# Optimization experiments

Hardware: AMD Instinct MI355X
Metric: run time of the kernel (lower is better)

## Reference

```python
import jax, jax.numpy as jnp
import numpy as np

K_DEPTH = 3
JAC_A = 1.0  # alpha (Jacobi a)
JAC_B = 1.0  # beta  (Jacobi b)


def jacobi_filter(sig, gammas):
    """Polynomial graph filter g(sigma) = sum_k gamma_k * P_k^{(a,b)}(sigma),
    Jacobi recurrence applied elementwise (Sigma is diagonal spectrum), domain [-1,1],
    fixed inner scalings (fixI=True => alphas=1)."""
    a, b = JAC_A, JAC_B
    xs = [jnp.ones_like(sig)]
    # L = 1
    coef1 = (a - b) / 2.0
    coef2 = (a + b + 2.0) / 2.0
    xs.append(coef1 * xs[0] + coef2 * sig * xs[0])
    for L in range(2, K_DEPTH + 1):
        cl = 2.0 * L * (L + a + b) * (2 * L - 2 + a + b)
        c1 = (2 * L + a + b - 1) * (2 * L + a + b) * (2 * L + a + b - 2)
        c2 = (2 * L + a + b - 1) * (a * a - b * b)
        c3 = 2.0 * (L - 1 + a) * (L - 1 + b) * (2 * L + a + b)
        xs.append((c1 / cl) * sig * xs[-1] - (c2 / cl) * xs[-1] - (c3 / cl) * xs[-2])
    basis = jnp.stack(xs, axis=0)  # [K+1, B, H, L, d]
    return jnp.einsum('k,kbhld->bhld', gammas, basis)


def setup_inputs() -> dict:
    key = jax.random.key(0)
    ks = jax.random.split(key, 7)
    B, L, Ha, Hs, d = 4, 2048, 4, 4, 64
    mk = lambda k, H: jax.random.normal(k, (B, L, H, d), dtype=jnp.float32)
    return {
        'U': mk(ks[0], Ha),
        'Sigma': mk(ks[1], Ha),
        'V': mk(ks[2], Ha),
        'values': mk(ks[3], Ha),
        'queries_softmax': mk(ks[4], Hs),
        'keys_softmax': mk(ks[5], Hs),
        'values_softmax': mk(ks[6], Hs),
        'gammas': jnp.ones((K_DEPTH + 1,), dtype=jnp.float32),
    }


def reference(U, Sigma, V, values, queries_softmax, keys_softmax, values_softmax, gammas):
    d_k = U.shape[-1]
    # ---- AGF (SVD) heads ----
    Uh = jax.nn.softmax(jnp.transpose(U, (0, 2, 1, 3)), axis=-1)        # [B,H,L,d]
    Vt = jax.nn.softmax(jnp.transpose(V, (0, 2, 3, 1)), axis=-1)        # [B,H,d,L]
    vals = jnp.transpose(values, (0, 2, 1, 3))                           # [B,H,L,d]
    sig = jax.nn.sigmoid(jnp.transpose(Sigma, (0, 2, 1, 3)))             # [B,H,L,d]
    gf = jacobi_filter(sig, gammas)                                       # [B,H,L,d]
    kv = jnp.einsum('bhdl,bhle->bhde', Vt, vals)                          # [B,H,d,d]
    out_agf = jnp.einsum('bhld,bhde->bhle', Uh * gf, kv)                  # [B,H,L,d]
    out_agf = jnp.transpose(out_agf, (0, 2, 1, 3))                        # [B,L,H,d]
    # ---- orthogonality loss ----
    eye = jnp.eye(d_k, dtype=Uh.dtype)
    sym_u = jnp.einsum('bhld,bhle->bhde', Uh, Uh) - eye
    sym_v = jnp.einsum('bhdl,bhel->bhde', Vt, Vt) - eye
    ortho_loss = jnp.mean(jnp.abs(sym_u), axis=(1, 2, 3)) + jnp.mean(jnp.abs(sym_v), axis=(1, 2, 3))
    # ---- softmax (flash) heads ----
    q = jnp.transpose(queries_softmax, (0, 2, 1, 3))
    k = jnp.transpose(keys_softmax, (0, 2, 1, 3))
    v = jnp.transpose(values_softmax, (0, 2, 1, 3))
    scores = jnp.einsum('bhld,bhsd->bhls', q, k) / jnp.sqrt(jnp.asarray(d_k, q.dtype))
    attn = jax.nn.softmax(scores, axis=-1)
    out_sm = jnp.einsum('bhls,bhsd->bhld', attn, v)
    out_sm = jnp.transpose(out_sm, (0, 2, 1, 3))                          # [B,L,H,d]
    out = jnp.concatenate([out_agf, out_sm], axis=2)                      # [B,L,2H,d]
    return out, ortho_loss
```

## Files before the change

kernel.cpp:

```cpp
#include <hip/hip_runtime.h>
#include <hip/hip_bf16.h>

#define BB 4
#define SEQ 2048
#define NH 4
#define D 64
#define NPAIR 16
#define HOUT 8
#define LOSS_BASE ((size_t)BB * SEQ * HOUT * D)

#define N_PART   (4 * 16 * 3 * 4096)
#define OFF_SPART N_PART
#define N_SPART  (16 * 32 * 64)
#define OFF_LPART (OFF_SPART + N_SPART)
#define N_LPART  (4 * 16 * 2048)
#define OFF_F32_END (OFF_LPART + N_LPART)
#define USZ ((size_t)16 * 2048 * 64)

typedef __attribute__((ext_vector_type(8))) short bf16x8;
typedef __attribute__((ext_vector_type(4))) float f32x4;
typedef __attribute__((ext_vector_type(8))) unsigned short us8;
typedef __attribute__((ext_vector_type(4))) unsigned short us4;

__device__ __forceinline__ unsigned short f2bf(float x) {
    union { float f; unsigned u; } v; v.f = x;
    unsigned r = v.u + 0x7fffu + ((v.u >> 16) & 1u);
    return (unsigned short)(r >> 16);
}
__device__ __forceinline__ float bf2f(unsigned short u) {
    union { unsigned u; float f; } v; v.u = ((unsigned)u) << 16; return v.f;
}
__device__ __forceinline__ unsigned cvt_pk_bf16(float lo, float hi) {
    unsigned r;
    asm("v_cvt_pk_bf16_f32 %0, %1, %2" : "=v"(r) : "v"(lo), "v"(hi));
    return r;
}
__device__ __forceinline__ void load16(const float* p, float* v) {
    const float4* q = (const float4*)p;
    float4 a = q[0], b = q[1], c = q[2], d = q[3];
    v[0]=a.x; v[1]=a.y; v[2]=a.z; v[3]=a.w;
    v[4]=b.x; v[5]=b.y; v[6]=b.z; v[7]=b.w;
    v[8]=c.x; v[9]=c.y; v[10]=c.z; v[11]=c.w;
    v[12]=d.x; v[13]=d.y; v[14]=d.z; v[15]=d.w;
}
__device__ __forceinline__ void wr_bf16x16(unsigned short* dst, const float* v) {
    unsigned w[8];
#pragma unroll
    for (int i = 0; i < 8; i++) w[i] = cvt_pk_bf16(v[2 * i], v[2 * i + 1]);
    *(uint4*)dst = make_uint4(w[0], w[1], w[2], w[3]);
    *(uint4*)(dst + 8) = make_uint4(w[4], w[5], w[6], w[7]);
}

__global__ __launch_bounds__(256) void prep(const float* __restrict__ U, const float* __restrict__ Sg,
                                            const float* __restrict__ Vagf, const float* __restrict__ vals,
                                            const float* __restrict__ Ksm, const float* __restrict__ Vsm,
                                            const float* __restrict__ gam,
                                            float* __restrict__ ws, unsigned short* __restrict__ usb,
                                            float* __restrict__ out) {
    int lt = blockIdx.x, p = blockIdx.y, stage = blockIdx.z;
    int b = p >> 2, h = p & 3;
    int tid = threadIdx.x;
    int r = tid >> 2;
    int c0 = (tid & 3) * 16;
    __shared__ float T[64][68];
    unsigned short* Khi   = usb;
    unsigned short* VbfT  = usb + USZ;
    unsigned short* UhT   = usb + 2 * USZ;
    unsigned short* EhiT  = usb + 3 * USZ;
    unsigned short* valsT = usb + 4 * USZ;
    unsigned short* Ughi  = usb + 5 * USZ;
    unsigned short* Uglo  = usb + 6 * USZ;
    float* Spart = ws + OFF_SPART;

    const size_t gbase = ((size_t)(b * SEQ + lt * 64 + r) * NH + h) * D + c0;
    const size_t nbase = ((size_t)(p * SEQ + lt * 64 + r)) * 64 + c0;
    const size_t tbase = ((size_t)p * 64 + r) * 2048 + lt * 64 + c0;
    float v[16], e[16];

    if (stage == 0) {
        load16(U + gbase, v);
        float mx = v[0];
#pragma unroll
        for (int k = 1; k < 16; k++) mx = fmaxf(mx, v[k]);
        mx = fmaxf(mx, __shfl_xor(mx, 1));
        mx = fmaxf(mx, __shfl_xor(mx, 2));
        float sm = 0.0f;
#pragma unroll
        for (int k = 0; k < 16; k++) { v[k] = __expf(v[k] - mx); sm += v[k]; }
        sm += __shfl_xor(sm, 1);
        sm += __shfl_xor(sm, 2);
        float inv = 1.0f / sm;
#pragma unroll
        for (int k = 0; k < 16; k++) { v[k] *= inv; T[r][c0 + k] = v[k]; }
        float sg[16];
        load16(Sg + gbase, sg);
        float g0 = gam[0], g1 = gam[1], g2 = gam[2], g3 = gam[3];
        us8 h0, h1, l0, l1;
#pragma unroll
        for (int k = 0; k < 16; k++) {
            float sig = 1.0f / (1.0f + __expf(-sg[k]));
            float x1 = 2.0f * sig;
            float x2 = 1.875f * sig * x1 - 0.75f;
            float x3 = 1.8666666666666667f * sig * x2 - 0.8f * x1;
            float ug = v[k] * (g0 + g1 * x1 + g2 * x2 + g3 * x3);
            unsigned short hh = f2bf(ug);
            unsigned short ll = f2bf(ug - bf2f(hh));
            if (k < 8) { h0[k] = hh; l0[k] = ll; } else { h1[k - 8] = hh; l1[k - 8] = ll; }
        }
        *(us8*)(Ughi + nbase) = h0; *(us8*)(Ughi + nbase + 8) = h1;
        *(us8*)(Uglo + nbase) = l0; *(us8*)(Uglo + nbase + 8) = l1;
        __syncthreads();
#pragma unroll
        for (int k = 0; k < 16; k++) e[k] = T[c0 + k][r];
        wr_bf16x16(UhT + tbase, e);
    } else if (stage == 1) {
        load16(Vagf + gbase, v);
#pragma unroll
        for (int k = 0; k < 16; k++) T[r][c0 + k] = __expf(v[k]);
        __syncthreads();
        float ssum = 0.0f;
#pragma unroll
        for (int k = 0; k < 16; k++) { e[k] = T[c0 + k][r]; ssum += e[k]; }
        ssum += __shfl_xor(ssum, 1);
        ssum += __shfl_xor(ssum, 2);
        if ((tid & 3) == 0) Spart[(p * 32 + lt) * 64 + r] = ssum;
        wr_bf16x16(EhiT + tbase, e);
    } else if (stage == 2) {
        load16(vals + gbase, v);
#pragma unroll
        for (int k = 0; k < 16; k++) T[r][c0 + k] = v[k];
        __syncthreads();
#pragma unroll
        for (int k = 0; k < 16; k++) e[k] = T[c0 + k][r];
        wr_bf16x16(valsT + tbase, e);
    } else if (stage == 3) {
        load16(Vsm + gbase, v);
#pragma unroll
        for (int k = 0; k < 16; k++) T[r][c0 + k] = v[k];
        __syncthreads();
#pragma unroll
        for (int k = 0; k < 16; k++) e[k] = T[c0 + k][r];
        wr_bf16x16(VbfT + tbase, e);
    } else {
        load16(Ksm + gbase, v);
        wr_bf16x16(Khi + nbase, v);
        if (lt == 0 && p == 0 && tid < BB) out[LOSS_BASE + tid] = 0.0f;
    }
}

#define PSTR 72
#define QSC 0.18033688011112042f

__global__ __launch_bounds__(256, 2) void mid(const unsigned short* __restrict__ usb,
                                              const float* __restrict__ Q,
                                              float* __restrict__ part,
                                              unsigned short* __restrict__ OpartUS,
                                              float* __restrict__ lpart) {
    __shared__ __align__(16) unsigned char smem[36864];
    const int bid = blockIdx.x;
    const int tid = threadIdx.x;
    const int w = tid >> 6, lane = tid & 63, lm = lane & 15, quad = lane >> 4;

    if (bid >= 64) {
        int fb = bid - 64;
        int qt2 = fb & 15, p = (fb >> 4) & 15, qr = fb >> 8;
        int b = p >> 2, h = p & 3;
        const unsigned short* Khi  = usb;
        const unsigned short* VbfT = usb + USZ;
        unsigned short* Kl = (unsigned short*)smem;
        unsigned short* Vl = Kl + 64 * PSTR;
        unsigned short* Ph = Vl + 64 * PSTR;
        const int srow = tid >> 2, sseg = (tid & 3) * 16;

        bf16x8 qhi[2][2], qlo[2][2];
#pragma unroll
        for (int q = 0; q < 2; q++) {
            int row = qt2 * 128 + q * 64 + w * 16 + lm;
            const float* qp = Q + ((size_t)(b * SEQ + row) * NH + h) * D + quad * 8;
#pragma unroll
            for (int ks = 0; ks < 2; ks++) {
                float qq[8];
                float4 a0 = *(const float4*)(qp + ks * 32);
                float4 a1 = *(const float4*)(qp + ks * 32 + 4);
                qq[0]=a0.x; qq[1]=a0.y; qq[2]=a0.z; qq[3]=a0.w;
                qq[4]=a1.x; qq[5]=a1.y; qq[6]=a1.z; qq[7]=a1.w;
#pragma unroll
                for (int j = 0; j < 8; j++) {
                    float xs = qq[j] * QSC;
                    unsigned short hi = f2bf(xs);
                    qhi[q][ks][j] = (short)hi;
                    qlo[q][ks][j] = (short)f2bf(xs - bf2f(hi));
                }
            }
        }

        float rsum[2] = {0.f, 0.f};
        f32x4 o[2][4];
#pragma unroll
        for (int q = 0; q < 2; q++)
#pragma unroll
            for (int t = 0; t < 4; t++) o[q][t] = (f32x4){0.f, 0.f, 0.f, 0.f};

        for (int kt = 0; kt < 8; ++kt) {
            __syncthreads();
            {
                size_t kb = ((size_t)(p * SEQ + qr * 512 + kt * 64 + srow)) * 64 + sseg;
                us8 k0 = *(const us8*)(Khi + kb);
                us8 k1 = *(const us8*)(Khi + kb + 8);
                size_t vb = ((size_t)p * 64 + srow) * 2048 + qr * 512 + kt * 64 + sseg;
                us8 v0 = *(const us8*)(VbfT + vb);
                us8 v1 = *(const us8*)(VbfT + vb + 8);
                *(us8*)&Kl[srow * PSTR + sseg] = k0; *(us8*)&Kl[srow * PSTR + sseg + 8] = k1;
                *(us8*)&Vl[srow * PSTR + sseg] = v0; *(us8*)&Vl[srow * PSTR + sseg + 8] = v1;
            }
            __syncthreads();

            bf16x8 kfr[4][2], vfr[4][2];
#pragma unroll
            for (int t = 0; t < 4; t++)
#pragma unroll
                for (int ks = 0; ks < 2; ks++) {
                    kfr[t][ks] = *(const bf16x8*)&Kl[(t * 16 + lm) * PSTR + ks * 32 + quad * 8];
                    vfr[t][ks] = *(const bf16x8*)&Vl[(t * 16 + lm) * PSTR + ks * 32 + quad * 8];
                }

#pragma unroll
            for (int q = 0; q < 2; q++) {
                unsigned short* Phq = Ph + (size_t)(w * 2 + q) * 16 * PSTR;
                f32x4 s[4];
#pragma unroll
                for (int t = 0; t < 4; t++) s[t] = (f32x4){0.f, 0.f, 0.f, 0.f};
#pragma unroll
                for (int t = 0; t < 4; t++)
#pragma unroll
                    for (int ks = 0; ks < 2; ks++) {
                        s[t] = __builtin_amdgcn_mfma_f32_16x16x32_bf16(kfr[t][ks], qhi[q][ks], s[t], 0, 0, 0);
                        s[t] = __builtin_amdgcn_mfma_f32_16x16x32_bf16(kfr[t][ks], qlo[q][ks], s[t], 0, 0, 0);
                    }
#pragma unroll
                for (int t = 0; t < 4; t++) {
                    float e0 = exp2f(s[t][0]);
                    float e1 = exp2f(s[t][1]);
                    float e2 = exp2f(s[t][2]);
                    float e3 = exp2f(s[t][3]);
                    rsum[q] += (e0 + e1) + (e2 + e3);
                    unsigned w0 = cvt_pk_bf16(e0, e1);
                    unsigned w1 = cvt_pk_bf16(e2, e3);
                    *(uint2*)&Phq[lm * PSTR + t * 16 + quad * 4] = make_uint2(w0, w1);
                }
                bf16x8 pf0 = *(const bf16x8*)&Phq[lm * PSTR + quad * 8];
                bf16x8 pf1 = *(const bf16x8*)&Phq[lm * PSTR + 32 + quad * 8];
#pragma unroll
                for (int dt = 0; dt < 4; dt++) {
                    o[q][dt] = __builtin_amdgcn_mfma_f32_16x16x32_bf16(vfr[dt][0], pf0, o[q][dt], 0, 0, 0);
                    o[q][dt] = __builtin_amdgcn_mfma_f32_16x16x32_bf16(vfr[dt][1], pf1, o[q][dt], 0, 0, 0);
                }
            }
        }

#pragma unroll
        for (int q = 0; q < 2; q++) {
            float rs = rsum[q];
            rs += __shfl_xor(rs, 16);
            rs += __shfl_xor(rs, 32);
            int qrow = qt2 * 128 + q * 64 + w * 16 + lm;
            size_t ob = ((size_t)(qr * 16 + p) * SEQ + qrow) * 64;
#pragma unroll
            for (int dt = 0; dt < 4; dt++) {
                unsigned w0 = cvt_pk_bf16(o[q][dt][0], o[q][dt][1]);
                unsigned w1 = cvt_pk_bf16(o[q][dt][2], o[q][dt][3]);
                *(uint2*)(OpartUS + ob + dt * 16 + quad * 4) = make_uint2(w0, w1);
            }
            if (quad == 0) lpart[(size_t)(qr * 16 + p) * SEQ + qrow] = rs;
        }
    } else {
        int split = bid >> 4, p = bid & 15;
        const unsigned short* UhT   = usb + 2 * USZ;
        const unsigned short* EhiT  = usb + 3 * USZ;
        const unsigned short* valsT = usb + 4 * USZ;
        unsigned short* Ut = (unsigned short*)smem;
        unsigned short* Eh = Ut + 64 * 40;
        unsigned short* Vt = Eh + 64 * 40;
        f32x4 su[4], sv[4], kv[4];
#pragma unroll
        for (int i = 0; i < 4; i++) { su[i] = (f32x4){0,0,0,0}; sv[i] = (f32x4){0,0,0,0}; kv[i] = (f32x4){0,0,0,0}; }
        int srow = tid >> 2;
        int sseg = (tid & 3) * 8;

        for (int step = 0; step < 16; ++step) {
            int l0 = split * 512 + step * 32;
            __syncthreads();
            size_t gb = ((size_t)p * 64 + srow) * 2048 + l0 + sseg;
            *(us8*)&Ut[srow * 40 + sseg] = *(const us8*)(UhT + gb);
            *(us8*)&Eh[srow * 40 + sseg] = *(const us8*)(EhiT + gb);
            *(us8*)&Vt[srow * 40 + sseg] = *(const us8*)(valsT + gb);
            __syncthreads();
            int ao = (w * 16 + lm) * 40 + quad * 8;
            bf16x8 au  = *(const bf16x8*)&Ut[ao];
            bf16x8 aeh = *(const bf16x8*)&Eh[ao];
#pragma unroll
            for (int nt = 0; nt < 4; nt++) {
                int bo = (nt * 16 + lm) * 40 + quad * 8;
                bf16x8 bu  = *(const bf16x8*)&Ut[bo];
                bf16x8 beh = *(const bf16x8*)&Eh[bo];
                bf16x8 bv  = *(const bf16x8*)&Vt[bo];
                su[nt] = __builtin_amdgcn_mfma_f32_16x16x32_bf16(au,  bu,  su[nt], 0, 0, 0);
                sv[nt] = __builtin_amdgcn_mfma_f32_16x16x32_bf16(aeh, beh, sv[nt], 0, 0, 0);
                kv[nt] = __builtin_amdgcn_mfma_f32_16x16x32_bf16(aeh, bv,  kv[nt], 0, 0, 0);
            }
        }
        float* dst = part + (size_t)(split * 16 + p) * 3 * 4096;
#pragma unroll
        for (int nt = 0; nt < 4; nt++)
#pragma unroll
            for (int reg = 0; reg < 4; reg++) {
                int off = (w * 16 + quad * 4 + reg) * 64 + nt * 16 + lm;
                dst[off] = su[nt][reg];
                dst[4096 + off] = sv[nt][reg];
                dst[8192 + off] = kv[nt][reg];
            }
    }
}

__global__ __launch_bounds__(256) void post(const float* __restrict__ part, const float* __restrict__ Spart,
                                            const unsigned short* __restrict__ usb,
                                            const unsigned short* __restrict__ OpartUS,
                                            const float* __restrict__ lpart, float* __restrict__ out) {
    const int bid = blockIdx.x;
    const int tid = threadIdx.x;
    if (bid < 2048) {
        int idx = bid * 256 + tid;
        int p = idx >> 15;
        int rem = idx & 32767;
        int l = rem >> 4, dq = rem & 15;
        int b = p >> 2, h = p & 3;
        f32x4 res = (f32x4){0.f, 0.f, 0.f, 0.f};
        float lsum = 0.0f;
#pragma unroll
        for (int qr = 0; qr < 4; qr++) {
            us4 a = *(const us4*)(OpartUS + ((size_t)(qr * 16 + p) * SEQ + l) * 64 + dq * 4);
            lsum += lpart[(size_t)(qr * 16 + p) * SEQ + l];
#pragma unroll
            for (int r = 0; r < 4; r++) res[r] += bf2f(a[r]);
        }
        float inv = 1.0f / lsum;
#pragma unroll
        for (int r = 0; r < 4; r++) res[r] *= inv;
        *(f32x4*)(out + ((size_t)(b * SEQ + l) * HOUT + 4 + h) * D + dq * 4) = res;
        return;
    }
    const int w = tid >> 6, lane = tid & 63, lm = lane & 15, quad = lane >> 4;
    int j = bid - 2048;
    int p = (j < 512) ? (j >> 5) : (j - 512);
    __shared__ float cis[64];
    __shared__ float red[4][64];
    __shared__ __align__(16) unsigned short KVh[64 * PSTR];
    __shared__ __align__(16) unsigned short KVl[64 * PSTR];
    {
        int d = tid & 63, grp = tid >> 6;
        float s = 0.0f;
#pragma unroll
        for (int i = 0; i < 8; i++) s += Spart[(p * 32 + grp * 8 + i) * 64 + d];
        red[grp][d] = s;
        __syncthreads();
        if (tid < 64) cis[tid] = 1.0f / (red[0][tid] + red[1][tid] + red[2][tid] + red[3][tid]);
        __syncthreads();
    }
    if (j >= 512) {
        float s = 0.0f;
        for (int idx = tid; idx < 8192; idx += 256) {
            int g = idx >> 12, i = idx & 4095;
            float v = 0.0f;
#pragma unroll
            for (int sp = 0; sp < 4; sp++) v += part[((size_t)(sp * 16 + p) * 3 + g) * 4096 + i];
            if (g) v *= cis[i >> 6] * cis[i & 63];
            float dg = ((i >> 6) == (i & 63)) ? 1.0f : 0.0f;
            s += fabsf(v - dg);
        }
#pragma unroll
        for (int o = 32; o > 0; o >>= 1) s += __shfl_xor(s, o);
        if ((tid & 63) == 0) red[0][(tid >> 6) * 2] = s;
        __syncthreads();
        if (tid == 0)
            atomicAdd(&out[LOSS_BASE + (p >> 2)],
                      (red[0][0] + red[0][2] + red[0][4] + red[0][6]) * (1.0f / 16384.0f));
        return;
    }
    int lt = j & 31;
    int b = p >> 2, h = p & 3;
    const unsigned short* Ughi = usb + 5 * USZ;
    const unsigned short* Uglo = usb + 6 * USZ;
    for (int idx = tid; idx < 4096; idx += 256) {
        int d = idx >> 6, e = idx & 63;
        float v = 0.0f;
#pragma unroll
        for (int sp = 0; sp < 4; sp++) v += part[((size_t)(sp * 16 + p) * 3 + 2) * 4096 + idx];
        v *= cis[d];
        unsigned short hh = f2bf(v);
        KVh[e * PSTR + d] = hh;
        KVl[e * PSTR + d] = f2bf(v - bf2f(hh));
    }
    __syncthreads();
    size_t ub = ((size_t)(p * SEQ + lt * 64 + w * 16 + lm)) * 64 + quad * 8;
    bf16x8 ah[2], al[2];
#pragma unroll
    for (int ks = 0; ks < 2; ks++) {
        ah[ks] = *(const bf16x8*)(Ughi + ub + ks * 32);
        al[ks] = *(const bf16x8*)(Uglo + ub + ks * 32);
    }
    f32x4 acc[4];
#pragma unroll
    for (int nt = 0; nt < 4; nt++) acc[nt] = (f32x4){0.f, 0.f, 0.f, 0.f};
#pragma unroll
    for (int nt = 0; nt < 4; nt++)
#pragma unroll
        for (int ks = 0; ks < 2; ks++) {
            bf16x8 bh = *(const bf16x8*)&KVh[(nt * 16 + lm) * PSTR + ks * 32 + quad * 8];
            bf16x8 bl = *(const bf16x8*)&KVl[(nt * 16 + lm) * PSTR + ks * 32 + quad * 8];
            acc[nt] = __builtin_amdgcn_mfma_f32_16x16x32_bf16(ah[ks], bh, acc[nt], 0, 0, 0);
            acc[nt] = __builtin_amdgcn_mfma_f32_16x16x32_bf16(al[ks], bh, acc[nt], 0, 0, 0);
            acc[nt] = __builtin_amdgcn_mfma_f32_16x16x32_bf16(ah[ks], bl, acc[nt], 0, 0, 0);
        }
#pragma unroll
    for (int nt = 0; nt < 4; nt++)
#pragma unroll
        for (int reg = 0; reg < 4; reg++)
            out[((size_t)(b * SEQ + lt * 64 + w * 16 + quad * 4 + reg) * HOUT + h) * D + nt * 16 + lm] =
                acc[nt][reg];
}

extern "C" void kernel_launch(void* const* d_in, const int* in_sizes, int n_in,
                              void* d_out, int out_size, void* d_ws, size_t ws_size,
                              hipStream_t stream) {
    (void)in_sizes; (void)n_in; (void)out_size; (void)ws_size;
    const float* U    = (const float*)d_in[0];
    const float* Sg   = (const float*)d_in[1];
    const float* V    = (const float*)d_in[2];
    const float* vals = (const float*)d_in[3];
    const float* Qs   = (const float*)d_in[4];
    const float* Ks   = (const float*)d_in[5];
    const float* Vv   = (const float*)d_in[6];
    const float* gam  = (const float*)d_in[7];
    float* out = (float*)d_out;

    float* ws = (float*)d_ws;
    float* part  = ws;
    float* Spart = ws + OFF_SPART;
    float* lpart = ws + OFF_LPART;
    unsigned short* usb = (unsigned short*)(ws + OFF_F32_END);
    unsigned short* OpartUS = usb + 7 * USZ;

    prep<<<dim3(32, 16, 5), 256, 0, stream>>>(U, Sg, V, vals, Ks, Vv, gam, ws, usb, out);
    mid<<<1088, 256, 0, stream>>>(usb, Qs, part, OpartUS, lpart);
    post<<<2576, 256, 0, stream>>>(part, Spart, usb, OpartUS, lpart, out);
}
```

Baseline: 169.9 us.

## Prefetch next K/V tiles into registers and add MFMA priority hints

Both branches of the mid kernel now load the next tile from global memory into registers while the current tile is consumed, so global latency overlaps compute. The __syncthreads calls become raw s_barrier plus an explicit lgkmcnt wait. The per-query P scratch is shared across the q loop, shrinking LDS from 36864 to 27648 bytes. s_setprio is raised around the MFMA blocks. The raw barriers and the reused P buffer carry ordering risk: if a wave writes P for q=1 before all its lanes have read P for q=0, results could be corrupted.

```diff
diff --git a/kernel.cpp b/kernel.cpp
--- a/kernel.cpp
+++ b/kernel.cpp
@@ -21,6 +21,9 @@
 typedef __attribute__((ext_vector_type(4))) float f32x4;
 typedef __attribute__((ext_vector_type(8))) unsigned short us8;
 typedef __attribute__((ext_vector_type(4))) unsigned short us4;
+
+#define BAR_PLAIN() asm volatile("s_barrier" ::: "memory")
+#define BAR_LGKM()  asm volatile("s_waitcnt lgkmcnt(0)\n\ts_barrier" ::: "memory")
 
 __device__ __forceinline__ unsigned short f2bf(float x) {
     union { float f; unsigned u; } v; v.f = x;
@@ -156,7 +159,7 @@
                                               float* __restrict__ part,
                                               unsigned short* __restrict__ OpartUS,
                                               float* __restrict__ lpart) {
-    __shared__ __align__(16) unsigned char smem[36864];
+    __shared__ __align__(16) unsigned char smem[27648];
     const int bid = blockIdx.x;
     const int tid = threadIdx.x;
     const int w = tid >> 6, lane = tid & 63, lm = lane & 15, quad = lane >> 4;
@@ -201,19 +204,29 @@
 #pragma unroll
             for (int t = 0; t < 4; t++) o[q][t] = (f32x4){0.f, 0.f, 0.f, 0.f};
 
+        us8 kr0, kr1, vr0, vr1;
+        {
+            size_t kb = ((size_t)(p * SEQ + qr * 512 + srow)) * 64 + sseg;
+            kr0 = *(const us8*)(Khi + kb);
+            kr1 = *(const us8*)(Khi + kb + 8);
+            size_t vb = ((size_t)p * 64 + srow) * 2048 + qr * 512 + sseg;
+            vr0 = *(const us8*)(VbfT + vb);
+            vr1 = *(const us8*)(VbfT + vb + 8);
+        }
+
         for (int kt = 0; kt < 8; ++kt) {
-            __syncthreads();
-            {
-                size_t kb = ((size_t)(p * SEQ + qr * 512 + kt * 64 + srow)) * 64 + sseg;
-                us8 k0 = *(const us8*)(Khi + kb);
-                us8 k1 = *(const us8*)(Khi + kb + 8);
-                size_t vb = ((size_t)p * 64 + srow) * 2048 + qr * 512 + kt * 64 + sseg;
-                us8 v0 = *(const us8*)(VbfT + vb);
-                us8 v1 = *(const us8*)(VbfT + vb + 8);
-                *(us8*)&Kl[srow * PSTR + sseg] = k0; *(us8*)&Kl[srow * PSTR + sseg + 8] = k1;
-                *(us8*)&Vl[srow * PSTR + sseg] = v0; *(us8*)&Vl[srow * PSTR + sseg + 8] = v1;
-            }
-            __syncthreads();
+            BAR_PLAIN();
+            *(us8*)&Kl[srow * PSTR + sseg] = kr0; *(us8*)&Kl[srow * PSTR + sseg + 8] = kr1;
+            *(us8*)&Vl[srow * PSTR + sseg] = vr0; *(us8*)&Vl[srow * PSTR + sseg + 8] = vr1;
+            if (kt < 7) {
+                size_t kb = ((size_t)(p * SEQ + qr * 512 + (kt + 1) * 64 + srow)) * 64 + sseg;
+                kr0 = *(const us8*)(Khi + kb);
+                kr1 = *(const us8*)(Khi + kb + 8);
+                size_t vb = ((size_t)p * 64 + srow) * 2048 + qr * 512 + (kt + 1) * 64 + sseg;
+                vr0 = *(const us8*)(VbfT + vb);
+                vr1 = *(const us8*)(VbfT + vb + 8);
+            }
+            BAR_LGKM();
 
             bf16x8 kfr[4][2], vfr[4][2];
 #pragma unroll
@@ -226,10 +239,11 @@
 
 #pragma unroll
             for (int q = 0; q < 2; q++) {
-                unsigned short* Phq = Ph + (size_t)(w * 2 + q) * 16 * PSTR;
+                unsigned short* Phq = Ph + (size_t)w * 16 * PSTR;
                 f32x4 s[4];
 #pragma unroll
                 for (int t = 0; t < 4; t++) s[t] = (f32x4){0.f, 0.f, 0.f, 0.f};
+                __builtin_amdgcn_s_setprio(1);
 #pragma unroll
                 for (int t = 0; t < 4; t++)
 #pragma unroll
@@ -237,6 +251,7 @@
                         s[t] = __builtin_amdgcn_mfma_f32_16x16x32_bf16(kfr[t][ks], qhi[q][ks], s[t], 0, 0, 0);
                         s[t] = __builtin_amdgcn_mfma_f32_16x16x32_bf16(kfr[t][ks], qlo[q][ks], s[t], 0, 0, 0);
                     }
+                __builtin_amdgcn_s_setprio(0);
 #pragma unroll
                 for (int t = 0; t < 4; t++) {
                     float e0 = exp2f(s[t][0]);
@@ -250,11 +265,13 @@
                 }
                 bf16x8 pf0 = *(const bf16x8*)&Phq[lm * PSTR + quad * 8];
                 bf16x8 pf1 = *(const bf16x8*)&Phq[lm * PSTR + 32 + quad * 8];
+                __builtin_amdgcn_s_setprio(1);
 #pragma unroll
                 for (int dt = 0; dt < 4; dt++) {
                     o[q][dt] = __builtin_amdgcn_mfma_f32_16x16x32_bf16(vfr[dt][0], pf0, o[q][dt], 0, 0, 0);
                     o[q][dt] = __builtin_amdgcn_mfma_f32_16x16x32_bf16(vfr[dt][1], pf1, o[q][dt], 0, 0, 0);
                 }
+                __builtin_amdgcn_s_setprio(0);
             }
         }
 
@@ -287,17 +304,30 @@
         int srow = tid >> 2;
         int sseg = (tid & 3) * 8;
 
+        us8 ur, er, vr;
+        {
+            size_t gb = ((size_t)p * 64 + srow) * 2048 + split * 512 + sseg;
+            ur = *(const us8*)(UhT + gb);
+            er = *(const us8*)(EhiT + gb);
+            vr = *(const us8*)(valsT + gb);
+        }
+
         for (int step = 0; step < 16; ++step) {
-            int l0 = split * 512 + step * 32;
-            __syncthreads();
-            size_t gb = ((size_t)p * 64 + srow) * 2048 + l0 + sseg;
-            *(us8*)&Ut[srow * 40 + sseg] = *(const us8*)(UhT + gb);
-            *(us8*)&Eh[srow * 40 + sseg] = *(const us8*)(EhiT + gb);
-            *(us8*)&Vt[srow * 40 + sseg] = *(const us8*)(valsT + gb);
-            __syncthreads();
+            BAR_PLAIN();
+            *(us8*)&Ut[srow * 40 + sseg] = ur;
+            *(us8*)&Eh[srow * 40 + sseg] = er;
+            *(us8*)&Vt[srow * 40 + sseg] = vr;
+            if (step < 15) {
+                size_t gb = ((size_t)p * 64 + srow) * 2048 + split * 512 + (step + 1) * 32 + sseg;
+                ur = *(const us8*)(UhT + gb);
+                er = *(const us8*)(EhiT + gb);
+                vr = *(const us8*)(valsT + gb);
+            }
+            BAR_LGKM();
             int ao = (w * 16 + lm) * 40 + quad * 8;
             bf16x8 au  = *(const bf16x8*)&Ut[ao];
             bf16x8 aeh = *(const bf16x8*)&Eh[ao];
+            __builtin_amdgcn_s_setprio(1);
 #pragma unroll
             for (int nt = 0; nt < 4; nt++) {
                 int bo = (nt * 16 + lm) * 40 + quad * 8;
@@ -308,6 +338,7 @@
                 sv[nt] = __builtin_amdgcn_mfma_f32_16x16x32_bf16(aeh, beh, sv[nt], 0, 0, 0);
                 kv[nt] = __builtin_amdgcn_mfma_f32_16x16x32_bf16(aeh, bv,  kv[nt], 0, 0, 0);
             }
+            __builtin_amdgcn_s_setprio(0);
         }
         float* dst = part + (size_t)(split * 16 + p) * 3 * 4096;
 #pragma unroll
```

New measurement: 173.2 us. About the same (+2.0%).

## Halve flash-attention KV split count and reorder post kernel block roles

Applied to the files above, without the earlier changes.

The softmax-head attention in the middle kernel now splits the key range into two halves of 1024 instead of four quarters of 512. Each block loops over 16 key tiles, so the grid shrinks from 1088 to 576 blocks and the partial output and row-sum traffic is halved. The post kernel combines two partials instead of four, and its block order changes so the AGF and loss blocks come first. The loss reduction is spread over four blocks per pair instead of one, and a shared-memory tile pad changes from 68 to 69. The cost is fewer, longer attention blocks, which may leave the GPU under-occupied.

```diff
diff --git a/kernel.cpp b/kernel.cpp
--- a/kernel.cpp
+++ b/kernel.cpp
@@ -13,7 +13,7 @@
 #define OFF_SPART N_PART
 #define N_SPART  (16 * 32 * 64)
 #define OFF_LPART (OFF_SPART + N_SPART)
-#define N_LPART  (4 * 16 * 2048)
+#define N_LPART  (2 * 16 * 2048)
 #define OFF_F32_END (OFF_LPART + N_LPART)
 #define USZ ((size_t)16 * 2048 * 64)
 
@@ -62,7 +62,7 @@
     int tid = threadIdx.x;
     int r = tid >> 2;
     int c0 = (tid & 3) * 16;
-    __shared__ float T[64][68];
+    __shared__ float T[64][69];
     unsigned short* Khi   = usb;
     unsigned short* VbfT  = usb + USZ;
     unsigned short* UhT   = usb + 2 * USZ;
@@ -163,7 +163,7 @@
 
     if (bid >= 64) {
         int fb = bid - 64;
-        int qt2 = fb & 15, p = (fb >> 4) & 15, qr = fb >> 8;
+        int qt2 = fb & 15, p = (fb >> 4) & 15, half = fb >> 8;
         int b = p >> 2, h = p & 3;
         const unsigned short* Khi  = usb;
         const unsigned short* VbfT = usb + USZ;
@@ -201,13 +201,13 @@
 #pragma unroll
             for (int t = 0; t < 4; t++) o[q][t] = (f32x4){0.f, 0.f, 0.f, 0.f};
 
-        for (int kt = 0; kt < 8; ++kt) {
+        for (int kt = 0; kt < 16; ++kt) {
             __syncthreads();
             {
-                size_t kb = ((size_t)(p * SEQ + qr * 512 + kt * 64 + srow)) * 64 + sseg;
+                size_t kb = ((size_t)(p * SEQ + half * 1024 + kt * 64 + srow)) * 64 + sseg;
                 us8 k0 = *(const us8*)(Khi + kb);
                 us8 k1 = *(const us8*)(Khi + kb + 8);
-                size_t vb = ((size_t)p * 64 + srow) * 2048 + qr * 512 + kt * 64 + sseg;
+                size_t vb = ((size_t)p * 64 + srow) * 2048 + half * 1024 + kt * 64 + sseg;
                 us8 v0 = *(const us8*)(VbfT + vb);
                 us8 v1 = *(const us8*)(VbfT + vb + 8);
                 *(us8*)&Kl[srow * PSTR + sseg] = k0; *(us8*)&Kl[srow * PSTR + sseg + 8] = k1;
@@ -264,14 +264,14 @@
             rs += __shfl_xor(rs, 16);
             rs += __shfl_xor(rs, 32);
             int qrow = qt2 * 128 + q * 64 + w * 16 + lm;
-            size_t ob = ((size_t)(qr * 16 + p) * SEQ + qrow) * 64;
+            size_t ob = ((size_t)(half * 16 + p) * SEQ + qrow) * 64;
 #pragma unroll
             for (int dt = 0; dt < 4; dt++) {
                 unsigned w0 = cvt_pk_bf16(o[q][dt][0], o[q][dt][1]);
                 unsigned w1 = cvt_pk_bf16(o[q][dt][2], o[q][dt][3]);
                 *(uint2*)(OpartUS + ob + dt * 16 + quad * 4) = make_uint2(w0, w1);
             }
-            if (quad == 0) lpart[(size_t)(qr * 16 + p) * SEQ + qrow] = rs;
+            if (quad == 0) lpart[(size_t)(half * 16 + p) * SEQ + qrow] = rs;
         }
     } else {
         int split = bid >> 4, p = bid & 15;
@@ -328,30 +328,23 @@
                                             const float* __restrict__ lpart, float* __restrict__ out) {
     const int bid = blockIdx.x;
     const int tid = threadIdx.x;
-    if (bid < 2048) {
-        int idx = bid * 256 + tid;
+    if (bid >= 576) {
+        int idx = (bid - 576) * 256 + tid;
         int p = idx >> 15;
         int rem = idx & 32767;
         int l = rem >> 4, dq = rem & 15;
         int b = p >> 2, h = p & 3;
-        f32x4 res = (f32x4){0.f, 0.f, 0.f, 0.f};
-        float lsum = 0.0f;
-#pragma unroll
-        for (int qr = 0; qr < 4; qr++) {
-            us4 a = *(const us4*)(OpartUS + ((size_t)(qr * 16 + p) * SEQ + l) * 64 + dq * 4);
-            lsum += lpart[(size_t)(qr * 16 + p) * SEQ + l];
-#pragma unroll
-            for (int r = 0; r < 4; r++) res[r] += bf2f(a[r]);
-        }
-        float inv = 1.0f / lsum;
-#pragma unroll
-        for (int r = 0; r < 4; r++) res[r] *= inv;
+        us4 a = *(const us4*)(OpartUS + ((size_t)p * SEQ + l) * 64 + dq * 4);
+        us4 c = *(const us4*)(OpartUS + ((size_t)(16 + p) * SEQ + l) * 64 + dq * 4);
+        float inv = 1.0f / (lpart[(size_t)p * SEQ + l] + lpart[(size_t)(16 + p) * SEQ + l]);
+        f32x4 res;
+#pragma unroll
+        for (int r = 0; r < 4; r++) res[r] = (bf2f(a[r]) + bf2f(c[r])) * inv;
         *(f32x4*)(out + ((size_t)(b * SEQ + l) * HOUT + 4 + h) * D + dq * 4) = res;
         return;
     }
     const int w = tid >> 6, lane = tid & 63, lm = lane & 15, quad = lane >> 4;
-    int j = bid - 2048;
-    int p = (j < 512) ? (j >> 5) : (j - 512);
+    int p = (bid < 512) ? (bid >> 5) : ((bid - 512) >> 2);
     __shared__ float cis[64];
     __shared__ float red[4][64];
     __shared__ __align__(16) unsigned short KVh[64 * PSTR];
@@ -366,9 +359,11 @@
         if (tid < 64) cis[tid] = 1.0f / (red[0][tid] + red[1][tid] + red[2][tid] + red[3][tid]);
         __syncthreads();
     }
-    if (j >= 512) {
+    if (bid >= 512) {
+        int chunk = (bid - 512) & 3;
         float s = 0.0f;
-        for (int idx = tid; idx < 8192; idx += 256) {
+        for (int t = 0; t < 8; t++) {
+            int idx = chunk * 2048 + t * 256 + tid;
             int g = idx >> 12, i = idx & 4095;
             float v = 0.0f;
 #pragma unroll
@@ -386,7 +381,7 @@
                       (red[0][0] + red[0][2] + red[0][4] + red[0][6]) * (1.0f / 16384.0f));
         return;
     }
-    int lt = j & 31;
+    int lt = bid & 31;
     int b = p >> 2, h = p & 3;
     const unsigned short* Ughi = usb + 5 * USZ;
     const unsigned short* Uglo = usb + 6 * USZ;
@@ -451,6 +446,6 @@
     unsigned short* OpartUS = usb + 7 * USZ;
 
     prep<<<dim3(32, 16, 5), 256, 0, stream>>>(U, Sg, V, vals, Ks, Vv, gam, ws, usb, out);
-    mid<<<1088, 256, 0, stream>>>(usb, Qs, part, OpartUS, lpart);
-    post<<<2576, 256, 0, stream>>>(part, Spart, usb, OpartUS, lpart, out);
-}
+    mid<<<576, 256, 0, stream>>>(usb, Qs, part, OpartUS, lpart);
+    post<<<2624, 256, 0, stream>>>(part, Spart, usb, OpartUS, lpart, out);
+}
```

Result: faster. 161.4 us (-5.0%).
